# Kernel tuning notes

Measured on AMD Instinct MI355X. Metric: run time of the kernel, lower is better.

Reference implementation:

```python
import jax, jax.numpy as jnp
import numpy as np

N, D_IN, HID, OUT, E = 131072, 256, 1024, 1, 100


def setup_inputs() -> dict:
    key = jax.random.key(0)
    k = jax.random.split(key, 7)
    return {
        "x": jax.random.normal(k[0], (N, D_IN), dtype=jnp.float32),
        "W1": jax.random.normal(k[1], (HID, D_IN), dtype=jnp.float32) * 0.05,
        "b1": jax.random.normal(k[2], (HID,), dtype=jnp.float32) * 0.05,
        "We": jax.random.normal(k[3], (E, OUT, HID), dtype=jnp.float32) * 0.05,
        "be": jax.random.normal(k[4], (E, OUT), dtype=jnp.float32) * 0.05,
        "num": jax.random.randint(k[5], (N,), 0, E, dtype=jnp.int64),
        "c": jax.random.randint(k[6], (E,), 0, E, dtype=jnp.int64),
    }


def reference(x, W1, b1, We, be, num, c):
    # feature: Linear + ReLU  -> [N, HID]
    h = jax.nn.relu(x @ W1.T + b1)
    # per-sample expert index: c[num[i]]
    e = c[num]                                  # [N]
    Wg = We[e]                                  # [N, OUT, HID] gathered expert weights
    bg = be[e]                                  # [N, OUT]
    y = jnp.einsum('noh,nh->no', Wg, h) + bg    # per-sample expert linear
    return jax.nn.sigmoid(y)
```

## Files before the change

### kernel.cpp

```cpp
#include <hip/hip_runtime.h>
#include <stdint.h>

#define N_SAMP 131072
#define DIN    256
#define HIDN   1024
#define BROWS  128
#define HCH    64
#define NCHUNK (HIDN / HCH)
#define LDSP   264

typedef __attribute__((ext_vector_type(8))) short short8;
typedef __attribute__((ext_vector_type(4))) float f32x4;

__device__ __forceinline__ unsigned short f2bf(float f) {
  unsigned u = __float_as_uint(f);
  u += 0x7fffu + ((u >> 16) & 1u);
  return (unsigned short)(u >> 16);
}

__device__ __forceinline__ short8 pack8(float4 a, float4 b) {
  short8 r;
  r[0] = (short)f2bf(a.x); r[1] = (short)f2bf(a.y);
  r[2] = (short)f2bf(a.z); r[3] = (short)f2bf(a.w);
  r[4] = (short)f2bf(b.x); r[5] = (short)f2bf(b.y);
  r[6] = (short)f2bf(b.z); r[7] = (short)f2bf(b.w);
  return r;
}

__global__ __launch_bounds__(256) void w1_to_bf16(const float* __restrict__ W1,
                                                  unsigned short* __restrict__ o) {
  int i = blockIdx.x * 256 + threadIdx.x;
  float4 f = ((const float4*)W1)[i];
  ushort4 v;
  v.x = f2bf(f.x); v.y = f2bf(f.y); v.z = f2bf(f.z); v.w = f2bf(f.w);
  ((ushort4*)o)[i] = v;
}

template <bool WBF>
__global__ __launch_bounds__(256, 3) void fused_kernel(
    const float* __restrict__ x,
    const float* __restrict__ W1f,
    const unsigned short* __restrict__ W1b,
    const float* __restrict__ b1,
    const float* __restrict__ We,
    const float* __restrict__ be,
    const int* __restrict__ num,
    const int* __restrict__ c,
    float* __restrict__ out)
{
  __shared__ unsigned short Wt[HCH * LDSP];
  __shared__ int e_sh[BROWS];

  const int tid  = threadIdx.x;
  const int lane = tid & 63;
  const int w    = tid >> 6;
  const int m    = lane & 15;
  const int quad = lane >> 4;
  const int R0   = blockIdx.x * BROWS;

  if (tid < BROWS) {
    int nv = num[R0 + tid];
    e_sh[tid] = c[nv];
  }

  short8 afr[2][8];
  {
    const float* xr0 = x + (size_t)(R0 + w * 32 + m) * DIN + quad * 8;
#pragma unroll
    for (int t = 0; t < 2; ++t) {
      const float* xr = xr0 + (size_t)t * 16 * DIN;
#pragma unroll
      for (int s = 0; s < 8; ++s) {
        float4 f0 = *(const float4*)(xr + s * 32);
        float4 f1 = *(const float4*)(xr + s * 32 + 4);
        afr[t][s] = pack8(f0, f1);
      }
    }
  }

  __syncthreads();

  int eid[2][4];
#pragma unroll
  for (int t = 0; t < 2; ++t)
#pragma unroll
    for (int r = 0; r < 4; ++r)
      eid[t][r] = e_sh[w * 32 + t * 16 + quad * 4 + r];

  float yacc[2][4] = {{0.f, 0.f, 0.f, 0.f}, {0.f, 0.f, 0.f, 0.f}};

  for (int ch = 0; ch < NCHUNK; ++ch) {
    const int hb = ch * HCH;

    if (WBF) {
      const uint4* Wg = (const uint4*)(W1b + (size_t)hb * DIN);
#pragma unroll
      for (int j = 0; j < 8; ++j) {
        int id = tid + j * 256;
        int r = id >> 5, kg = id & 31;
        uint4 v = Wg[id];
        *(uint4*)&Wt[r * LDSP + kg * 8] = v;
      }
    } else {
      const float4* Wg = (const float4*)(W1f + (size_t)hb * DIN);
#pragma unroll
      for (int j = 0; j < 8; ++j) {
        int id = tid + j * 256;
        int r = id >> 5, kg = id & 31;
        float4 f0 = Wg[id * 2];
        float4 f1 = Wg[id * 2 + 1];
        short8 v = pack8(f0, f1);
        *(short8*)&Wt[r * LDSP + kg * 8] = v;
      }
    }
    __syncthreads();

    f32x4 acc[2][4];
#pragma unroll
    for (int t = 0; t < 2; ++t)
#pragma unroll
      for (int nt = 0; nt < 4; ++nt)
        acc[t][nt] = (f32x4){0.f, 0.f, 0.f, 0.f};

#pragma unroll
    for (int s = 0; s < 8; ++s) {
      short8 bfr[4];
#pragma unroll
      for (int nt = 0; nt < 4; ++nt)
        bfr[nt] = *(const short8*)&Wt[(nt * 16 + m) * LDSP + s * 32 + quad * 8];
#pragma unroll
      for (int t = 0; t < 2; ++t)
#pragma unroll
        for (int nt = 0; nt < 4; ++nt)
          acc[t][nt] = __builtin_amdgcn_mfma_f32_16x16x32_bf16(
              afr[t][s], bfr[nt], acc[t][nt], 0, 0, 0);
    }
    __syncthreads();

#pragma unroll
    for (int nt = 0; nt < 4; ++nt) {
      int col = hb + nt * 16 + m;
      float bv = b1[col];
      const float* Wec = We + col;
#pragma unroll
      for (int t = 0; t < 2; ++t)
#pragma unroll
        for (int r = 0; r < 4; ++r) {
          float h = acc[t][nt][r] + bv;
          h = fmaxf(h, 0.f);
          yacc[t][r] = fmaf(h, Wec[(size_t)eid[t][r] * HIDN], yacc[t][r]);
        }
    }
  }

#pragma unroll
  for (int t = 0; t < 2; ++t)
#pragma unroll
    for (int r = 0; r < 4; ++r) {
      float v = yacc[t][r];
      v += __shfl_xor(v, 1);
      v += __shfl_xor(v, 2);
      v += __shfl_xor(v, 4);
      v += __shfl_xor(v, 8);
      yacc[t][r] = v;
    }

  if (m == 0) {
#pragma unroll
    for (int t = 0; t < 2; ++t)
#pragma unroll
      for (int r = 0; r < 4; ++r) {
        int row = R0 + w * 32 + t * 16 + quad * 4 + r;
        float yy = yacc[t][r] + be[eid[t][r]];
        out[row] = 1.f / (1.f + __expf(-yy));
      }
  }
}

extern "C" void kernel_launch(void* const* d_in, const int* in_sizes, int n_in,
                              void* d_out, int out_size, void* d_ws, size_t ws_size,
                              hipStream_t stream) {
  const float* x   = (const float*)d_in[0];
  const float* W1  = (const float*)d_in[1];
  const float* b1  = (const float*)d_in[2];
  const float* We  = (const float*)d_in[3];
  const float* be  = (const float*)d_in[4];
  const int*   num = (const int*)d_in[5];
  const int*   c   = (const int*)d_in[6];
  float* out = (float*)d_out;

  const size_t w1bf_bytes = (size_t)HIDN * DIN * sizeof(unsigned short);
  const bool usebf = ws_size >= w1bf_bytes;
  unsigned short* w1bf = (unsigned short*)d_ws;

  if (usebf) {
    w1_to_bf16<<<dim3((HIDN * DIN / 4) / 256), dim3(256), 0, stream>>>(W1, w1bf);
    fused_kernel<true><<<dim3(N_SAMP / BROWS), dim3(256), 0, stream>>>(
        x, W1, w1bf, b1, We, be, num, c, out);
  } else {
    fused_kernel<false><<<dim3(N_SAMP / BROWS), dim3(256), 0, stream>>>(
        x, W1, w1bf, b1, We, be, num, c, out);
  }
}
```

Measured before the change: 304.4 us.

## Double rows per block to amortize W1 tile loads across more samples

Each block now handles 256 rows, with each wave keeping 64 rows of x in registers as bf16 fragments, so every W1 chunk staged in LDS is reused by twice as many samples. To bound accumulator registers, the MFMA and epilogue are split into two 32-column halves, and the epilogue for each half runs before the second barrier. Expert row offsets are precomputed as eid*HIDN. The aim is to halve global/LDS traffic for W1 per sample, at the cost of higher register pressure, occupancy lowered to 2 blocks per CU, and half as many blocks.

After: 347.1 us. +14.0%, slower.

```diff
diff --git a/kernel.cpp b/kernel.cpp
--- a/kernel.cpp
+++ b/kernel.cpp
@@ -4,7 +4,7 @@
 #define N_SAMP 131072
 #define DIN    256
 #define HIDN   1024
-#define BROWS  128
+#define BROWS  256
 #define HCH    64
 #define NCHUNK (HIDN / HCH)
 #define LDSP   264
@@ -37,7 +37,7 @@
 }
 
 template <bool WBF>
-__global__ __launch_bounds__(256, 3) void fused_kernel(
+__global__ __launch_bounds__(256, 2) void fused_kernel(
     const float* __restrict__ x,
     const float* __restrict__ W1f,
     const unsigned short* __restrict__ W1b,
@@ -57,17 +57,15 @@
   const int m    = lane & 15;
   const int quad = lane >> 4;
   const int R0   = blockIdx.x * BROWS;
-
-  if (tid < BROWS) {
-    int nv = num[R0 + tid];
-    e_sh[tid] = c[nv];
-  }
-
-  short8 afr[2][8];
+  const int rb   = w * 64;
+
+  e_sh[tid] = c[num[R0 + tid]];
+
+  short8 afr[4][8];
   {
-    const float* xr0 = x + (size_t)(R0 + w * 32 + m) * DIN + quad * 8;
-#pragma unroll
-    for (int t = 0; t < 2; ++t) {
+    const float* xr0 = x + (size_t)(R0 + rb + m) * DIN + quad * 8;
+#pragma unroll
+    for (int t = 0; t < 4; ++t) {
       const float* xr = xr0 + (size_t)t * 16 * DIN;
 #pragma unroll
       for (int s = 0; s < 8; ++s) {
@@ -80,14 +78,18 @@
 
   __syncthreads();
 
-  int eid[2][4];
-#pragma unroll
-  for (int t = 0; t < 2; ++t)
+  int eoff[4][4];
+#pragma unroll
+  for (int t = 0; t < 4; ++t)
 #pragma unroll
     for (int r = 0; r < 4; ++r)
-      eid[t][r] = e_sh[w * 32 + t * 16 + quad * 4 + r];
-
-  float yacc[2][4] = {{0.f, 0.f, 0.f, 0.f}, {0.f, 0.f, 0.f, 0.f}};
+      eoff[t][r] = e_sh[rb + t * 16 + quad * 4 + r] * HIDN;
+
+  float yacc[4][4];
+#pragma unroll
+  for (int t = 0; t < 4; ++t)
+#pragma unroll
+    for (int r = 0; r < 4; ++r) yacc[t][r] = 0.f;
 
   for (int ch = 0; ch < NCHUNK; ++ch) {
     const int hb = ch * HCH;
@@ -115,46 +117,49 @@
     }
     __syncthreads();
 
-    f32x4 acc[2][4];
-#pragma unroll
-    for (int t = 0; t < 2; ++t)
-#pragma unroll
-      for (int nt = 0; nt < 4; ++nt)
-        acc[t][nt] = (f32x4){0.f, 0.f, 0.f, 0.f};
-
-#pragma unroll
-    for (int s = 0; s < 8; ++s) {
-      short8 bfr[4];
-#pragma unroll
-      for (int nt = 0; nt < 4; ++nt)
-        bfr[nt] = *(const short8*)&Wt[(nt * 16 + m) * LDSP + s * 32 + quad * 8];
-#pragma unroll
-      for (int t = 0; t < 2; ++t)
-#pragma unroll
-        for (int nt = 0; nt < 4; ++nt)
-          acc[t][nt] = __builtin_amdgcn_mfma_f32_16x16x32_bf16(
-              afr[t][s], bfr[nt], acc[t][nt], 0, 0, 0);
+#pragma unroll
+    for (int hf = 0; hf < 2; ++hf) {
+      f32x4 acc[4][2];
+#pragma unroll
+      for (int t = 0; t < 4; ++t)
+#pragma unroll
+        for (int j = 0; j < 2; ++j)
+          acc[t][j] = (f32x4){0.f, 0.f, 0.f, 0.f};
+
+#pragma unroll
+      for (int s = 0; s < 8; ++s) {
+        short8 bfr[2];
+#pragma unroll
+        for (int j = 0; j < 2; ++j)
+          bfr[j] = *(const short8*)&Wt[(hf * 32 + j * 16 + m) * LDSP + s * 32 + quad * 8];
+#pragma unroll
+        for (int t = 0; t < 4; ++t)
+#pragma unroll
+          for (int j = 0; j < 2; ++j)
+            acc[t][j] = __builtin_amdgcn_mfma_f32_16x16x32_bf16(
+                afr[t][s], bfr[j], acc[t][j], 0, 0, 0);
+      }
+
+#pragma unroll
+      for (int j = 0; j < 2; ++j) {
+        int col = hb + hf * 32 + j * 16 + m;
+        float bv = b1[col];
+        const float* Wec = We + col;
+#pragma unroll
+        for (int t = 0; t < 4; ++t)
+#pragma unroll
+          for (int r = 0; r < 4; ++r) {
+            float h = acc[t][j][r] + bv;
+            h = fmaxf(h, 0.f);
+            yacc[t][r] = fmaf(h, Wec[eoff[t][r]], yacc[t][r]);
+          }
+      }
     }
     __syncthreads();
-
-#pragma unroll
-    for (int nt = 0; nt < 4; ++nt) {
-      int col = hb + nt * 16 + m;
-      float bv = b1[col];
-      const float* Wec = We + col;
-#pragma unroll
-      for (int t = 0; t < 2; ++t)
-#pragma unroll
-        for (int r = 0; r < 4; ++r) {
-          float h = acc[t][nt][r] + bv;
-          h = fmaxf(h, 0.f);
-          yacc[t][r] = fmaf(h, Wec[(size_t)eid[t][r] * HIDN], yacc[t][r]);
-        }
-    }
-  }
-
-#pragma unroll
-  for (int t = 0; t < 2; ++t)
+  }
+
+#pragma unroll
+  for (int t = 0; t < 4; ++t)
 #pragma unroll
     for (int r = 0; r < 4; ++r) {
       float v = yacc[t][r];
@@ -166,14 +171,16 @@
     }
 
   if (m == 0) {
-#pragma unroll
-    for (int t = 0; t < 2; ++t)
+    const int ebase = rb + quad * 4;
+#pragma unroll
+    for (int t = 0; t < 4; ++t)
 #pragma unroll
       for (int r = 0; r < 4; ++r) {
-        int row = R0 + w * 32 + t * 16 + quad * 4 + r;
-        float yy = yacc[t][r] + be[eid[t][r]];
+        int row = R0 + rb + t * 16 + quad * 4 + r;
+        float yy = yacc[t][r] + be[eoff[t][r] / HIDN];
         out[row] = 1.f / (1.f + __expf(-yy));
       }
+    (void)ebase;
   }
 }
 
```

## Double-buffer W1 chunks in LDS with async global_load_lds and XOR swizzle

Applied to the files above, without the earlier changes.

Replaces the single padded LDS tile with two unpadded XOR-swizzled buffers. The next W1 chunk is prefetched with direct global-to-LDS loads while MFMAs run on the current chunk, which cuts one barrier per chunk. The intent is to overlap weight loading with compute and avoid LDS bank conflicts without padding. The price is twice the LDS footprint, and launch bounds drop from 3 to 2 blocks per SIMD, which lowers occupancy.

After: 260.9 us. -14.3%, faster.

```diff
diff --git a/kernel.cpp b/kernel.cpp
--- a/kernel.cpp
+++ b/kernel.cpp
@@ -5,9 +5,7 @@
 #define DIN    256
 #define HIDN   1024
 #define BROWS  128
-#define HCH    64
-#define NCHUNK (HIDN / HCH)
-#define LDSP   264
+#define NCHUNK 16
 
 typedef __attribute__((ext_vector_type(8))) short short8;
 typedef __attribute__((ext_vector_type(4))) float f32x4;
@@ -37,7 +35,7 @@
 }
 
 template <bool WBF>
-__global__ __launch_bounds__(256, 3) void fused_kernel(
+__global__ __launch_bounds__(256, 2) void fused_kernel(
     const float* __restrict__ x,
     const float* __restrict__ W1f,
     const unsigned short* __restrict__ W1b,
@@ -48,24 +46,21 @@
     const int* __restrict__ c,
     float* __restrict__ out)
 {
-  __shared__ unsigned short Wt[HCH * LDSP];
+  __shared__ unsigned short Wt[2][64 * DIN];
   __shared__ int e_sh[BROWS];
 
   const int tid  = threadIdx.x;
   const int lane = tid & 63;
   const int w    = tid >> 6;
-  const int m    = lane & 15;
+  const int n    = lane & 15;
   const int quad = lane >> 4;
   const int R0   = blockIdx.x * BROWS;
 
-  if (tid < BROWS) {
-    int nv = num[R0 + tid];
-    e_sh[tid] = c[nv];
-  }
+  if (tid < BROWS) e_sh[tid] = c[num[R0 + tid]];
 
   short8 afr[2][8];
   {
-    const float* xr0 = x + (size_t)(R0 + w * 32 + m) * DIN + quad * 8;
+    const float* xr0 = x + (size_t)(R0 + w * 32 + n) * DIN + quad * 8;
 #pragma unroll
     for (int t = 0; t < 2; ++t) {
       const float* xr = xr0 + (size_t)t * 16 * DIN;
@@ -78,43 +73,78 @@
     }
   }
 
+  const int h2 = lane >> 5;
+  const int p  = lane & 31;
+
+  if (WBF) {
+#pragma unroll
+    for (int j = 0; j < 8; ++j) {
+      int inst = w * 8 + j;
+      int r = inst * 2 + h2;
+      int kg = p ^ ((r & 7) << 2);
+      const unsigned short* g = W1b + (r << 8) + (kg << 3);
+      __builtin_amdgcn_global_load_lds(
+          (const __attribute__((address_space(1))) unsigned int*)g,
+          (__attribute__((address_space(3))) unsigned int*)(&Wt[0][0] + inst * 512),
+          16, 0, 0);
+    }
+  } else {
+#pragma unroll
+    for (int j = 0; j < 8; ++j) {
+      int id = tid + j * 256;
+      int r = id >> 5, pp = id & 31;
+      int kg = pp ^ ((r & 7) << 2);
+      const float* gs = W1f + (r << 8) + (kg << 3);
+      float4 f0 = *(const float4*)gs;
+      float4 f1 = *(const float4*)(gs + 4);
+      *(short8*)&Wt[0][r * DIN + pp * 8] = pack8(f0, f1);
+    }
+  }
+
   __syncthreads();
 
-  int eid[2][4];
+  int eoff[2][4];
 #pragma unroll
   for (int t = 0; t < 2; ++t)
 #pragma unroll
     for (int r = 0; r < 4; ++r)
-      eid[t][r] = e_sh[w * 32 + t * 16 + quad * 4 + r];
+      eoff[t][r] = e_sh[w * 32 + t * 16 + quad * 4 + r] * HIDN;
 
   float yacc[2][4] = {{0.f, 0.f, 0.f, 0.f}, {0.f, 0.f, 0.f, 0.f}};
 
+  int buf = 0;
   for (int ch = 0; ch < NCHUNK; ++ch) {
-    const int hb = ch * HCH;
-
-    if (WBF) {
-      const uint4* Wg = (const uint4*)(W1b + (size_t)hb * DIN);
-#pragma unroll
-      for (int j = 0; j < 8; ++j) {
-        int id = tid + j * 256;
-        int r = id >> 5, kg = id & 31;
-        uint4 v = Wg[id];
-        *(uint4*)&Wt[r * LDSP + kg * 8] = v;
+    if (ch + 1 < NCHUNK) {
+      if (WBF) {
+        const unsigned short* Wg = W1b + (size_t)(ch + 1) * (64 * DIN);
+        unsigned short* db = &Wt[buf ^ 1][0];
+#pragma unroll
+        for (int j = 0; j < 8; ++j) {
+          int inst = w * 8 + j;
+          int r = inst * 2 + h2;
+          int kg = p ^ ((r & 7) << 2);
+          const unsigned short* g = Wg + (r << 8) + (kg << 3);
+          __builtin_amdgcn_global_load_lds(
+              (const __attribute__((address_space(1))) unsigned int*)g,
+              (__attribute__((address_space(3))) unsigned int*)(db + inst * 512),
+              16, 0, 0);
+        }
+      } else {
+        const float* Wg = W1f + (size_t)(ch + 1) * (64 * DIN);
+#pragma unroll
+        for (int j = 0; j < 8; ++j) {
+          int id = tid + j * 256;
+          int r = id >> 5, pp = id & 31;
+          int kg = pp ^ ((r & 7) << 2);
+          const float* gs = Wg + (r << 8) + (kg << 3);
+          float4 f0 = *(const float4*)gs;
+          float4 f1 = *(const float4*)(gs + 4);
+          *(short8*)&Wt[buf ^ 1][r * DIN + pp * 8] = pack8(f0, f1);
+        }
       }
-    } else {
-      const float4* Wg = (const float4*)(W1f + (size_t)hb * DIN);
-#pragma unroll
-      for (int j = 0; j < 8; ++j) {
-        int id = tid + j * 256;
-        int r = id >> 5, kg = id & 31;
-        float4 f0 = Wg[id * 2];
-        float4 f1 = Wg[id * 2 + 1];
-        short8 v = pack8(f0, f1);
-        *(short8*)&Wt[r * LDSP + kg * 8] = v;
-      }
-    }
-    __syncthreads();
-
+    }
+
+    const unsigned short* WtB = &Wt[buf][0];
     f32x4 acc[2][4];
 #pragma unroll
     for (int t = 0; t < 2; ++t)
@@ -124,10 +154,11 @@
 
 #pragma unroll
     for (int s = 0; s < 8; ++s) {
+      const int F = (s * 4 + quad) ^ ((n & 7) << 2);
       short8 bfr[4];
 #pragma unroll
       for (int nt = 0; nt < 4; ++nt)
-        bfr[nt] = *(const short8*)&Wt[(nt * 16 + m) * LDSP + s * 32 + quad * 8];
+        bfr[nt] = *(const short8*)&WtB[(nt * 16 + n) * DIN + F * 8];
 #pragma unroll
       for (int t = 0; t < 2; ++t)
 #pragma unroll
@@ -135,11 +166,10 @@
           acc[t][nt] = __builtin_amdgcn_mfma_f32_16x16x32_bf16(
               afr[t][s], bfr[nt], acc[t][nt], 0, 0, 0);
     }
-    __syncthreads();
 
 #pragma unroll
     for (int nt = 0; nt < 4; ++nt) {
-      int col = hb + nt * 16 + m;
+      int col = ch * 64 + nt * 16 + n;
       float bv = b1[col];
       const float* Wec = We + col;
 #pragma unroll
@@ -148,9 +178,12 @@
         for (int r = 0; r < 4; ++r) {
           float h = acc[t][nt][r] + bv;
           h = fmaxf(h, 0.f);
-          yacc[t][r] = fmaf(h, Wec[(size_t)eid[t][r] * HIDN], yacc[t][r]);
+          yacc[t][r] = fmaf(h, Wec[eoff[t][r]], yacc[t][r]);
         }
     }
+
+    __syncthreads();
+    buf ^= 1;
   }
 
 #pragma unroll
@@ -165,13 +198,13 @@
       yacc[t][r] = v;
     }
 
-  if (m == 0) {
+  if (n == 0) {
 #pragma unroll
     for (int t = 0; t < 2; ++t)
 #pragma unroll
       for (int r = 0; r < 4; ++r) {
         int row = R0 + w * 32 + t * 16 + quad * 4 + r;
-        float yy = yacc[t][r] + be[eid[t][r]];
+        float yy = yacc[t][r] + be[eoff[t][r] >> 10];
         out[row] = 1.f / (1.f + __expf(-yy));
       }
   }
```
